# Performance work log

Measured on AMD Instinct MI355X. Metric: run time of the kernel, lower is better.

The kernel has to match this reference:

```python
import jax, jax.numpy as jnp
import numpy as np

B, S, E, P, K, H = 32, 512, 1024, 256, 3, 8
KERNELS = 4  # conv repeated KERNELS times then averaged -> identical to a single conv


def setup_inputs() -> dict:
    key = jax.random.key(0)
    ks = jax.random.split(key, 8)
    sc = 0.02
    x = jax.random.normal(ks[0], (B, S, E), jnp.float32)
    # lengths must satisfy 3 <= l <= S-1 so slice [1:l+1] and conv length l-2 are valid
    seq_length = jax.random.randint(ks[1], (B,), 16, S - 1)
    proj_w = jax.random.normal(ks[2], (E, P), jnp.float32) * sc
    proj_b = jnp.zeros((P,), jnp.float32)
    conv_w = jax.random.normal(ks[3], (P, P, K), jnp.float32) * sc  # (out, in, width)
    conv_b = jnp.zeros((P,), jnp.float32)
    attn_w = jax.random.normal(ks[4], (P, H * S), jnp.float32) * sc
    attn_b = jnp.zeros((H * S,), jnp.float32)
    c1_w = jax.random.normal(ks[5], (P, P // 2), jnp.float32) * sc
    c1_b = jnp.zeros((P // 2,), jnp.float32)
    c2_w = jax.random.normal(ks[6], (P // 2, 2), jnp.float32) * sc
    c2_b = jnp.zeros((2,), jnp.float32)
    return dict(x=x, seq_length=seq_length, proj_w=proj_w, proj_b=proj_b,
                conv_w=conv_w, conv_b=conv_b, attn_w=attn_w, attn_b=attn_b,
                c1_w=c1_w, c1_b=c1_b, c2_w=c2_w, c2_b=c2_b)


def _forward(x, seq_length, proj_w, proj_b, conv_w, conv_b, attn_w, attn_b,
             c1_w, c1_b, c2_w, c2_b):
    # projection: (B,S,E) -> (B,S,P)
    proj = jnp.einsum('bse,ep->bsp', x, proj_w) + proj_b
    proj_pc = jnp.transpose(proj, (0, 2, 1))  # (B,P,S)
    # original convs each sample over slice [1:l+1]; conv is local, so conv the
    # full slice [1:] once and mask invalid tail positions per sample.
    conv = jax.lax.conv_general_dilated(
        proj_pc[:, :, 1:], conv_w, window_strides=(1,), padding='VALID',
        dimension_numbers=('NCH', 'OIH', 'NCH'))  # (B,P,S-K)
    conv = jax.nn.relu(conv + conv_b[None, :, None])
    # sum of KERNELS identical relu(conv) outputs divided by KERNELS == conv (identity)
    m = S - K  # conv output length over slice [1:]
    l = seq_length[:, None]  # (B,1)
    valid = jnp.arange(m)[None, :] < (l - (K - 1))  # output j valid iff j < l-2
    conv = jnp.where(valid[:, None, :], conv, 0.0)
    # pad: position 0 zero, conv outputs at 1..l-2, zeros after -> (B,P,S)
    rep_conv = jnp.zeros((B, P, S), conv.dtype).at[:, :, 1:1 + m].set(conv)
    rep_conv = jnp.transpose(rep_conv, (0, 2, 1))  # (B,S,P)
    # attention: logits (B,S,H*S), softmax over the FULL H*S axis (original dim=1)
    logits = jnp.einsum('bsp,pk->bsk', rep_conv, attn_w) + attn_b
    attn = jax.nn.softmax(logits, axis=-1).reshape(B, S, H, S)
    # per sample: mean over heads, sum over query rows -> weights over key pos q
    w = attn.sum(axis=(1, 2)) / H  # (B,S)
    rep_attn = jnp.einsum('bq,bqp->bp', w, rep_conv)  # (B,P)
    h = jnp.einsum('bp,ph->bh', rep_attn, c1_w) + c1_b
    h = jnp.where(h > 0, h, 0.01 * h)  # LeakyReLU(0.01)
    cls = jnp.einsum('bh,hc->bc', h, c2_w) + c2_b
    return jax.nn.softmax(cls, axis=-1)


def reference(x, seq_length, proj_w, proj_b, conv_w, conv_b, attn_w, attn_b,
              c1_w, c1_b, c2_w, c2_b):
    probs = _forward(x, seq_length, proj_w, proj_b, conv_w, conv_b,
                     attn_w, attn_b, c1_w, c1_b, c2_w, c2_b)
    return probs, jnp.argmax(probs, axis=1)
```

## Files before the change

kernel.cpp:

```cpp
#include <hip/hip_runtime.h>
#include <hip/hip_fp8.h>

#define B_ 32
#define S_ 512
#define E_ 1024
#define P_ 256
#define HH 8

typedef __attribute__((ext_vector_type(8))) short bf16x8;
typedef __attribute__((ext_vector_type(8))) unsigned short us8;
typedef __attribute__((ext_vector_type(4))) unsigned short us4;
typedef __attribute__((ext_vector_type(16))) float f32x16;
typedef __attribute__((ext_vector_type(4))) float f32x4;
typedef __attribute__((ext_vector_type(8))) unsigned char u8x8;

#define SA 8.0f
#define SB 16.0f
#define SINV (1.0f / 128.0f)
#define LOG2E 1.44269504088896f
#define SINV2 (SINV * LOG2E)

static __device__ __forceinline__ unsigned short f2bf(float f) {
  union { float f; unsigned int u; } v;
  v.f = f;
  unsigned int r = (v.u + 0x7FFFu + ((v.u >> 16) & 1u)) >> 16;
  return (unsigned short)r;
}
static __device__ __forceinline__ float bf2f(unsigned short u) {
  union { unsigned int u; float f; } v;
  v.u = ((unsigned int)u) << 16;
  return v.f;
}
static __device__ __forceinline__ unsigned char f2fp8(float f) {
  return (unsigned char)__hip_cvt_float_to_fp8(f, __HIP_SATFINITE, __HIP_E4M3);
}

__global__ __launch_bounds__(256) void k_prep(const float* __restrict__ pw,
                                              const float* __restrict__ cw,
                                              const float* __restrict__ aw,
                                              unsigned short* __restrict__ pwB,
                                              unsigned short* __restrict__ wtB,
                                              unsigned char* __restrict__ awB8,
                                              float* __restrict__ zbase) {
  int bid = blockIdx.x;
  int t = threadIdx.x;
  if (bid < 160) {
    zbase[bid * 256 + t] = 0.f;
    return;
  }
  bid -= 160;
  if (bid < 128) {
    int g = bid >> 4, kc = (bid & 15) * 4 + (t >> 6);
    int l = t & 63;
    int n = g * 32 + (l & 31);
    int kbase = kc * 16 + (l >> 5) * 8;
    us8 v;
#pragma unroll
    for (int j = 0; j < 8; j++) v[j] = f2bf(pw[(size_t)(kbase + j) * P_ + n]);
    *(us8*)(pwB + ((size_t)g * 64 + kc) * 512 + l * 8) = v;
    return;
  }
  bid -= 128;
  if (bid < 96) {
    int g = bid / 12, kidx = (bid % 12) * 4 + (t >> 6);
    int l = t & 63;
    int o = g * 32 + (l & 31);
    int xb = kidx * 16 + (l >> 5) * 8;
    us8 v;
#pragma unroll
    for (int j = 0; j < 8; j++) {
      int x = xb + j;
      int k = x >> 8, i = x & 255;
      v[j] = f2bf(cw[(size_t)o * 768 + i * 3 + k]);
    }
    *(us8*)(wtB + ((size_t)g * 48 + kidx) * 512 + l * 8) = v;
    return;
  }
  bid -= 96;
  {
    int g = bid >> 1, ks = (bid & 1) * 4 + (t >> 6);
    int l = t & 63;
    int j0 = g * 16 + (l & 15);
    int kbase = ks * 32 + (l >> 4) * 8;
    u8x8 v;
#pragma unroll
    for (int j = 0; j < 8; j++) v[j] = f2fp8(aw[(size_t)(kbase + j) * 4096 + j0] * SB);
    *(u8x8*)(awB8 + ((size_t)g * 8 + ks) * 512 + l * 8) = v;
  }
}

__global__ __launch_bounds__(256) void k_swz8(const unsigned short* __restrict__ src,
                                              unsigned char* __restrict__ dst) {
  int g = blockIdx.x, ks = blockIdx.y * 4 + (threadIdx.x >> 6);
  int l = threadIdx.x & 63;
  us8 v = *(const us8*)(src + (size_t)(g * 16 + (l & 15)) * 256 + ks * 32 + (l >> 4) * 8);
  u8x8 o;
#pragma unroll
  for (int j = 0; j < 8; j++) o[j] = f2fp8(bf2f(v[j]) * SA);
  *(u8x8*)(dst + ((size_t)g * 8 + ks) * 512 + l * 8) = o;
}

__global__ __launch_bounds__(512) void k_proj_mfma(const float* __restrict__ x,
                                                   const unsigned short* __restrict__ pwB,
                                                   const float* __restrict__ pb,
                                                   unsigned short* __restrict__ proj16) {
  __shared__ unsigned short As[16 * 64 * 8];
  const int m0 = blockIdx.x * 64;
  const int t = threadIdx.x;
  const int w = t >> 6, lane = t & 63, ln31 = lane & 31, kh = lane >> 5;
  const int c0 = w * 32;

  f32x16 acc0, acc1;
#pragma unroll
  for (int r = 0; r < 16; r++) { acc0[r] = 0.f; acc1[r] = 0.f; }

  const unsigned short* bp = pwB + (size_t)w * 64 * 512 + lane * 8;

  for (int kc = 0; kc < E_; kc += 128) {
#pragma unroll
    for (int i = 0; i < 4; i++) {
      int c = t + i * 512;
      int row = c >> 5, pos = c & 31;
      float4 v = *(const float4*)(x + (size_t)(m0 + row) * E_ + kc + pos * 4);
      us4 h;
      h[0] = f2bf(v.x); h[1] = f2bf(v.y); h[2] = f2bf(v.z); h[3] = f2bf(v.w);
      *(us4*)&As[((pos >> 1) * 64 + row) * 8 + (pos & 1) * 4] = h;
    }
    __syncthreads();
    const int kcs = kc >> 4;
#pragma unroll
    for (int kk = 0; kk < 8; kk++) {
      bf16x8 a0 = *(const bf16x8*)&As[((2 * kk + kh) * 64 + ln31) * 8];
      bf16x8 a1 = *(const bf16x8*)&As[((2 * kk + kh) * 64 + 32 + ln31) * 8];
      bf16x8 b  = *(const bf16x8*)(bp + (size_t)(kcs + kk) * 512);
      acc0 = __builtin_amdgcn_mfma_f32_32x32x16_bf16(a0, b, acc0, 0, 0, 0);
      acc1 = __builtin_amdgcn_mfma_f32_32x32x16_bf16(a1, b, acc1, 0, 0, 0);
    }
    __syncthreads();
  }
  float pbv = pb[c0 + ln31];
#pragma unroll
  for (int r = 0; r < 16; r++) {
    int rl = (r & 3) + 8 * (r >> 2) + 4 * kh;
    proj16[(size_t)(m0 + rl) * P_ + c0 + ln31]      = f2bf(acc0[r] + pbv);
    proj16[(size_t)(m0 + 32 + rl) * P_ + c0 + ln31] = f2bf(acc1[r] + pbv);
  }
}

__global__ __launch_bounds__(512) void k_conv_mfma(const unsigned short* __restrict__ proj16,
                                                   const unsigned short* __restrict__ wtB,
                                                   const float* __restrict__ cb,
                                                   const int* __restrict__ seq,
                                                   unsigned short* __restrict__ rep16) {
  __shared__ unsigned short As[32 * 66 * 8];
  const int m0 = blockIdx.x * 64;
  const int bb = m0 >> 9, s0 = m0 & 511;
  const int t = threadIdx.x;
  const int w = t >> 6, lane = t & 63, ln31 = lane & 31, kh = lane >> 5;
  const int c0 = w * 32;

#pragma unroll
  for (int i = 0; i < 5; i++) {
    int c = t + i * 512;
    if (c < 2112) {
      int row = c >> 5, kk2 = c & 31;
      us8 v = {0, 0, 0, 0, 0, 0, 0, 0};
      if (s0 + row <= 511)
        v = *(const us8*)(proj16 + (size_t)(bb * S_ + s0 + row) * P_ + kk2 * 8);
      *(us8*)&As[(kk2 * 66 + row) * 8] = v;
    }
  }
  __syncthreads();

  f32x16 acc0, acc1;
#pragma unroll
  for (int r = 0; r < 16; r++) { acc0[r] = 0.f; acc1[r] = 0.f; }

  const unsigned short* bbase = wtB + (size_t)w * 48 * 512 + lane * 8;

#pragma unroll
  for (int k = 0; k < 3; k++) {
#pragma unroll
    for (int kk = 0; kk < 16; kk++) {
      bf16x8 a0 = *(const bf16x8*)&As[((2 * kk + kh) * 66 + k + ln31) * 8];
      bf16x8 a1 = *(const bf16x8*)&As[((2 * kk + kh) * 66 + k + 32 + ln31) * 8];
      bf16x8 b  = *(const bf16x8*)(bbase + (size_t)(k * 16 + kk) * 512);
      acc0 = __builtin_amdgcn_mfma_f32_32x32x16_bf16(a0, b, acc0, 0, 0, 0);
      acc1 = __builtin_amdgcn_mfma_f32_32x32x16_bf16(a1, b, acc1, 0, 0, 0);
    }
  }

  int l = seq[bb];
  float cbv = cb[c0 + ln31];
#pragma unroll
  for (int r = 0; r < 16; r++) {
    int rl = (r & 3) + 8 * (r >> 2) + 4 * kh;
    int s_a = s0 + rl, s_b = s0 + 32 + rl;
    float ma = (s_a >= 1 && s_a <= 509 && s_a < l - 1) ? 1.f : 0.f;
    float mb = (s_b >= 1 && s_b <= 509 && s_b < l - 1) ? 1.f : 0.f;
    rep16[(size_t)(m0 + rl) * P_ + c0 + ln31]      = f2bf(fmaxf(acc0[r] + cbv, 0.f) * ma);
    rep16[(size_t)(m0 + 32 + rl) * P_ + c0 + ln31] = f2bf(fmaxf(acc1[r] + cbv, 0.f) * mb);
  }
}

__global__ __launch_bounds__(256) void k_attn_mfma(const unsigned char* __restrict__ repF8,
                                                   const unsigned char* __restrict__ awB8,
                                                   const float* __restrict__ ab,
                                                   unsigned short* __restrict__ E16,
                                                   float* __restrict__ Z) {
  __shared__ __align__(16) unsigned char As8[16384];
  const int m0 = blockIdx.x * 64;
  const int q0 = blockIdx.y * 128;
  const int t = threadIdx.x;
  const int w = t >> 6, lane = t & 63;
  const int ln15 = lane & 15, l4 = lane >> 4;

  {
    const float4* src = (const float4*)(repF8 + (size_t)m0 * 256);
    float4* dst = (float4*)As8;
#pragma unroll
    for (int i = 0; i < 4; i++) dst[t + i * 256] = src[t + i * 256];
  }
  __syncthreads();

  const int qg = (q0 >> 5) + w;

  f32x4 ef[8];
#pragma unroll
  for (int i = 0; i < 8; i++) ef[i] = (f32x4){0.f, 0.f, 0.f, 0.f};

#pragma unroll 1
  for (int h = 0; h < HH; h++) {
    unsigned oz = 0;
    asm volatile("" : "+v"(oz));
    const unsigned char* bh = awB8 + (size_t)(h * 32 + qg * 2) * 8 * 512 + lane * 8;
    f32x4 acc[8];
#pragma unroll
    for (int i = 0; i < 8; i++) acc[i] = (f32x4){0.f, 0.f, 0.f, 0.f};
#pragma unroll
    for (int ks = 0; ks < 8; ks++) {
      long b0 = *(const long*)(bh + (size_t)ks * 512);
      long b1 = *(const long*)(bh + (size_t)(8 + ks) * 512);
#pragma unroll
      for (int rt = 0; rt < 4; rt++) {
        long a = *(const long*)&As8[(rt * 8 + ks) * 512 + lane * 8 + oz];
        acc[rt * 2 + 0] = __builtin_amdgcn_mfma_f32_16x16x32_fp8_fp8(a, b0, acc[rt * 2 + 0], 0, 0, 0);
        acc[rt * 2 + 1] = __builtin_amdgcn_mfma_f32_16x16x32_fp8_fp8(a, b1, acc[rt * 2 + 1], 0, 0, 0);
      }
    }
    float bias0 = ab[h * 512 + qg * 32 + ln15] * LOG2E;
    float bias1 = ab[h * 512 + qg * 32 + 16 + ln15] * LOG2E;
#pragma unroll
    for (int rt = 0; rt < 4; rt++)
#pragma unroll
      for (int r = 0; r < 4; r++) {
        ef[rt * 2 + 0][r] += __builtin_amdgcn_exp2f(acc[rt * 2 + 0][r] * SINV2 + bias0);
        ef[rt * 2 + 1][r] += __builtin_amdgcn_exp2f(acc[rt * 2 + 1][r] * SINV2 + bias1);
      }
  }

#pragma unroll
  for (int rt = 0; rt < 4; rt++)
#pragma unroll
    for (int r = 0; r < 4; r++) {
      int row = m0 + rt * 16 + l4 * 4 + r;
      E16[(size_t)row * 512 + qg * 32 + ln15]      = f2bf(ef[rt * 2 + 0][r]);
      E16[(size_t)row * 512 + qg * 32 + 16 + ln15] = f2bf(ef[rt * 2 + 1][r]);
    }

#pragma unroll
  for (int rt = 0; rt < 4; rt++)
#pragma unroll
    for (int r = 0; r < 4; r++) {
      float z = ef[rt * 2 + 0][r] + ef[rt * 2 + 1][r];
#pragma unroll
      for (int st = 8; st >= 1; st >>= 1) z += __shfl_xor(z, st, 64);
      if (ln15 == 0) atomicAdd(&Z[m0 + rt * 16 + l4 * 4 + r], z);
    }
}

__global__ __launch_bounds__(512) void k_w(const unsigned short* __restrict__ E16,
                                           const float* __restrict__ Z,
                                           float* __restrict__ wB) {
  __shared__ float rZ[64];
  int b = blockIdx.x, c = blockIdx.y, t = threadIdx.x;
  int s0 = c * 64;
  if (t < 64) rZ[t] = 1.0f / Z[b * 512 + s0 + t];
  __syncthreads();
  float acc = 0.f;
#pragma unroll 8
  for (int s = 0; s < 64; s++)
    acc += bf2f(E16[(size_t)(b * 512 + s0 + s) * 512 + t]) * rZ[s];
  atomicAdd(&wB[b * 512 + t], acc * (1.0f / HH));
}

__global__ __launch_bounds__(256) void k_final_a(const unsigned short* __restrict__ rep16,
                                                 const float* __restrict__ wB,
                                                 float* __restrict__ repA) {
  __shared__ float wS[64];
  int b = blockIdx.x, qc = blockIdx.y, t = threadIdx.x;
  if (t < 64) wS[t] = wB[b * 512 + qc * 64 + t];
  __syncthreads();
  int p0 = (t & 63) * 4, qo = t >> 6;
  float a0 = 0.f, a1 = 0.f, a2 = 0.f, a3 = 0.f;
  for (int q = qo; q < 64; q += 4) {
    us4 v = *(const us4*)(rep16 + (size_t)(b * 512 + qc * 64 + q) * 256 + p0);
    float wq = wS[q];
    a0 += wq * bf2f(v[0]); a1 += wq * bf2f(v[1]);
    a2 += wq * bf2f(v[2]); a3 += wq * bf2f(v[3]);
  }
  atomicAdd(&repA[b * 256 + p0 + 0], a0);
  atomicAdd(&repA[b * 256 + p0 + 1], a1);
  atomicAdd(&repA[b * 256 + p0 + 2], a2);
  atomicAdd(&repA[b * 256 + p0 + 3], a3);
}

__global__ __launch_bounds__(128) void k_final_b(const float* __restrict__ repA,
                                                 const float* __restrict__ c1w,
                                                 const float* __restrict__ c1b,
                                                 const float* __restrict__ c2w,
                                                 const float* __restrict__ c2b,
                                                 float* __restrict__ out) {
  __shared__ float hS[128];
  __shared__ float clsS[2];
  int b = blockIdx.x, t = threadIdx.x;
  float acc = c1b[t];
  for (int p = 0; p < 256; p++) acc += repA[b * 256 + p] * c1w[p * 128 + t];
  hS[t] = acc > 0.f ? acc : 0.01f * acc;
  __syncthreads();
  if (t < 2) {
    float a2 = c2b[t];
    for (int j = 0; j < 128; j++) a2 += hS[j] * c2w[j * 2 + t];
    clsS[t] = a2;
  }
  __syncthreads();
  if (t == 0) {
    float c0 = clsS[0], c1 = clsS[1];
    float m = fmaxf(c0, c1);
    float e0 = __expf(c0 - m), e1 = __expf(c1 - m);
    float inv = 1.0f / (e0 + e1);
    float p0 = e0 * inv, p1 = e1 * inv;
    out[b * 2 + 0] = p0;
    out[b * 2 + 1] = p1;
    out[B_ * 2 + b] = (p1 > p0) ? 1.0f : 0.0f;
  }
}

extern "C" void kernel_launch(void* const* d_in, const int* in_sizes, int n_in,
                              void* d_out, int out_size, void* d_ws, size_t ws_size,
                              hipStream_t stream) {
  const float* x   = (const float*)d_in[0];
  const int*   seq = (const int*)d_in[1];
  const float* pw  = (const float*)d_in[2];
  const float* pb  = (const float*)d_in[3];
  const float* cw  = (const float*)d_in[4];
  const float* cb  = (const float*)d_in[5];
  const float* aw  = (const float*)d_in[6];
  const float* ab  = (const float*)d_in[7];
  const float* c1w = (const float*)d_in[8];
  const float* c1b = (const float*)d_in[9];
  const float* c2w = (const float*)d_in[10];
  const float* c2b = (const float*)d_in[11];
  float* out = (float*)d_out;

  char* ws = (char*)d_ws;
  unsigned short* proj16 = (unsigned short*)(ws);
  unsigned short* E16    = (unsigned short*)(ws);
  unsigned short* rep16  = (unsigned short*)(ws + (size_t)16777216);
  unsigned char*  repF8  = (unsigned char*)(ws + (size_t)25165824);
  unsigned char*  awB8   = (unsigned char*)(ws + (size_t)29360128);
  unsigned short* pwB    = (unsigned short*)(ws + (size_t)30408704);
  unsigned short* wtB    = (unsigned short*)(ws + (size_t)30932992);
  float*          Z      = (float*)(ws + (size_t)31326208);
  float*          wB     = (float*)(ws + (size_t)31391744);
  float*          repA   = (float*)(ws + (size_t)31457280);

  k_prep<<<896, 256, 0, stream>>>(pw, cw, aw, pwB, wtB, awB8, Z);
  k_proj_mfma<<<256, 512, 0, stream>>>(x, pwB, pb, proj16);
  k_conv_mfma<<<256, 512, 0, stream>>>(proj16, wtB, cb, seq, rep16);
  k_swz8<<<dim3(1024, 2), 256, 0, stream>>>(rep16, repF8);
  k_attn_mfma<<<dim3(256, 4), 256, 0, stream>>>(repF8, awB8, ab, E16, Z);
  k_w<<<dim3(32, 8), 512, 0, stream>>>(E16, Z, wB);
  k_final_a<<<dim3(32, 8), 256, 0, stream>>>(rep16, wB, repA);
  k_final_b<<<32, 128, 0, stream>>>(repA, c1w, c1b, c2w, c2b, out);
}
```

Measured before the change: 213.9 us.

## Double-buffer attention weight tiles in LDS via async global_load_lds prefetch

The attention MFMA kernel now stages each head's fp8 weight slice into a double-buffered shared-memory area using direct global-to-LDS loads. It prefetches the next head's slice while the current head's MFMAs run, with per-wave `s_waitcnt vmcnt` gating instead of block barriers. The per-head bias values are also loaded into registers once before the loop. This is meant to hide global-load latency on the B operand. In exchange the kernel takes 64KB of extra LDS, which lowers occupancy, and the bias array is indexed by a runtime loop counter, which may force it into scratch or indexed register moves.

Result: no change. 216.4 us (+1.2%).

```diff
diff --git a/kernel.cpp b/kernel.cpp
--- a/kernel.cpp
+++ b/kernel.cpp
@@ -33,6 +33,11 @@
 }
 static __device__ __forceinline__ unsigned char f2fp8(float f) {
   return (unsigned char)__hip_cvt_float_to_fp8(f, __HIP_SATFINITE, __HIP_E4M3);
+}
+static __device__ __forceinline__ void gll16(const void* g, void* l) {
+  __builtin_amdgcn_global_load_lds(
+      (const __attribute__((address_space(1))) void*)g,
+      (__attribute__((address_space(3))) void*)l, 16, 0, 0);
 }
 
 __global__ __launch_bounds__(256) void k_prep(const float* __restrict__ pw,
@@ -209,11 +214,13 @@
                                                    unsigned short* __restrict__ E16,
                                                    float* __restrict__ Z) {
   __shared__ __align__(16) unsigned char As8[16384];
+  __shared__ __align__(16) unsigned char Bs[2][32768];
   const int m0 = blockIdx.x * 64;
   const int q0 = blockIdx.y * 128;
   const int t = threadIdx.x;
   const int w = t >> 6, lane = t & 63;
   const int ln15 = lane & 15, l4 = lane >> 4;
+  const int qg = (q0 >> 5) + w;
 
   {
     const float4* src = (const float4*)(repF8 + (size_t)m0 * 256);
@@ -221,9 +228,22 @@
 #pragma unroll
     for (int i = 0; i < 4; i++) dst[t + i * 256] = src[t + i * 256];
   }
-  __syncthreads();
-
-  const int qg = (q0 >> 5) + w;
+
+  float biasr[2][8];
+#pragma unroll
+  for (int h = 0; h < HH; h++) {
+    biasr[0][h] = ab[h * 512 + qg * 32 + ln15] * LOG2E;
+    biasr[1][h] = ab[h * 512 + qg * 32 + 16 + ln15] * LOG2E;
+    asm volatile("" : "+v"(biasr[0][h]), "+v"(biasr[1][h]));
+  }
+
+  {
+    const unsigned char* bs = awB8 + (size_t)(qg * 2) * 4096 + lane * 16;
+    unsigned char* bd = &Bs[0][0] + w * 8192;
+#pragma unroll
+    for (int i = 0; i < 8; i++) gll16(bs + i * 1024, bd + i * 1024);
+  }
+  __syncthreads();
 
   f32x4 ef[8];
 #pragma unroll
@@ -231,16 +251,27 @@
 
 #pragma unroll 1
   for (int h = 0; h < HH; h++) {
+    if (h < HH - 1) {
+      const unsigned char* bs = awB8 + (size_t)((h + 1) * 32 + qg * 2) * 4096 + lane * 16;
+      unsigned char* bd = &Bs[(h + 1) & 1][0] + w * 8192;
+#pragma unroll
+      for (int i = 0; i < 8; i++) gll16(bs + i * 1024, bd + i * 1024);
+      asm volatile("s_waitcnt vmcnt(8)" ::: "memory");
+    } else {
+      asm volatile("s_waitcnt vmcnt(0)" ::: "memory");
+    }
+    __builtin_amdgcn_sched_barrier(0);
+
     unsigned oz = 0;
     asm volatile("" : "+v"(oz));
-    const unsigned char* bh = awB8 + (size_t)(h * 32 + qg * 2) * 8 * 512 + lane * 8;
+    const unsigned char* bh = &Bs[h & 1][0] + w * 8192 + lane * 8;
     f32x4 acc[8];
 #pragma unroll
     for (int i = 0; i < 8; i++) acc[i] = (f32x4){0.f, 0.f, 0.f, 0.f};
 #pragma unroll
     for (int ks = 0; ks < 8; ks++) {
-      long b0 = *(const long*)(bh + (size_t)ks * 512);
-      long b1 = *(const long*)(bh + (size_t)(8 + ks) * 512);
+      long b0 = *(const long*)(bh + ks * 512);
+      long b1 = *(const long*)(bh + 4096 + ks * 512);
 #pragma unroll
       for (int rt = 0; rt < 4; rt++) {
         long a = *(const long*)&As8[(rt * 8 + ks) * 512 + lane * 8 + oz];
@@ -248,8 +279,8 @@
         acc[rt * 2 + 1] = __builtin_amdgcn_mfma_f32_16x16x32_fp8_fp8(a, b1, acc[rt * 2 + 1], 0, 0, 0);
       }
     }
-    float bias0 = ab[h * 512 + qg * 32 + ln15] * LOG2E;
-    float bias1 = ab[h * 512 + qg * 32 + 16 + ln15] * LOG2E;
+    float bias0 = biasr[0][h];
+    float bias1 = biasr[1][h];
 #pragma unroll
     for (int rt = 0; rt < 4; rt++)
 #pragma unroll
```

## Double-buffer projection GEMM A tile with register prefetch and XOR-swizzled LDS

Applied to the files above, without the earlier changes.

The projection kernel now prefetches the next 128-wide K chunk of x into registers while MFMAs consume the current LDS buffer. It then converts that chunk to bf16 and writes it into a second LDS buffer, leaving one barrier per iteration instead of two. The LDS layout also gains an XOR swizzle meant to reduce bank conflicts on the writes and the MFMA operand reads. The cost is double the LDS footprint and more live registers, which could lower occupancy.

After: 226.5 us. 1.06x slower.

```diff
diff --git a/kernel.cpp b/kernel.cpp
--- a/kernel.cpp
+++ b/kernel.cpp
@@ -100,44 +100,80 @@
   *(u8x8*)(dst + ((size_t)g * 8 + ks) * 512 + l * 8) = o;
 }
 
+static __device__ __forceinline__ int aidx(int q, int row, int half) {
+  return (((q * 64 + row) * 8) + half * 4) ^ (((q ^ (row >> 3)) & 7) << 3);
+}
+
 __global__ __launch_bounds__(512) void k_proj_mfma(const float* __restrict__ x,
                                                    const unsigned short* __restrict__ pwB,
                                                    const float* __restrict__ pb,
                                                    unsigned short* __restrict__ proj16) {
-  __shared__ unsigned short As[16 * 64 * 8];
+  __shared__ unsigned short As[2][16 * 64 * 8];
   const int m0 = blockIdx.x * 64;
   const int t = threadIdx.x;
   const int w = t >> 6, lane = t & 63, ln31 = lane & 31, kh = lane >> 5;
   const int c0 = w * 32;
+  const int rbase = t >> 5, pos = t & 31;
+  const int q = pos >> 1, half = pos & 1;
 
   f32x16 acc0, acc1;
 #pragma unroll
   for (int r = 0; r < 16; r++) { acc0[r] = 0.f; acc1[r] = 0.f; }
 
   const unsigned short* bp = pwB + (size_t)w * 64 * 512 + lane * 8;
-
-  for (int kc = 0; kc < E_; kc += 128) {
-#pragma unroll
-    for (int i = 0; i < 4; i++) {
-      int c = t + i * 512;
-      int row = c >> 5, pos = c & 31;
-      float4 v = *(const float4*)(x + (size_t)(m0 + row) * E_ + kc + pos * 4);
-      us4 h;
-      h[0] = f2bf(v.x); h[1] = f2bf(v.y); h[2] = f2bf(v.z); h[3] = f2bf(v.w);
-      *(us4*)&As[((pos >> 1) * 64 + row) * 8 + (pos & 1) * 4] = h;
-    }
-    __syncthreads();
-    const int kcs = kc >> 4;
+  const float* xbase = x + (size_t)(m0 + rbase) * E_ + pos * 4;
+
+  float4 v0, v1, v2, v3;
+  v0 = *(const float4*)(xbase);
+  v1 = *(const float4*)(xbase + 16 * E_);
+  v2 = *(const float4*)(xbase + 32 * E_);
+  v3 = *(const float4*)(xbase + 48 * E_);
+  {
+    us4 h;
+    h[0] = f2bf(v0.x); h[1] = f2bf(v0.y); h[2] = f2bf(v0.z); h[3] = f2bf(v0.w);
+    *(us4*)&As[0][aidx(q, rbase, half)] = h;
+    h[0] = f2bf(v1.x); h[1] = f2bf(v1.y); h[2] = f2bf(v1.z); h[3] = f2bf(v1.w);
+    *(us4*)&As[0][aidx(q, rbase + 16, half)] = h;
+    h[0] = f2bf(v2.x); h[1] = f2bf(v2.y); h[2] = f2bf(v2.z); h[3] = f2bf(v2.w);
+    *(us4*)&As[0][aidx(q, rbase + 32, half)] = h;
+    h[0] = f2bf(v3.x); h[1] = f2bf(v3.y); h[2] = f2bf(v3.z); h[3] = f2bf(v3.w);
+    *(us4*)&As[0][aidx(q, rbase + 48, half)] = h;
+  }
+  __syncthreads();
+
+  for (int k8 = 0; k8 < 8; k8++) {
+    const int cur = k8 & 1;
+    if (k8 < 7) {
+      const float* xs = xbase + (k8 + 1) * 128;
+      v0 = *(const float4*)(xs);
+      v1 = *(const float4*)(xs + 16 * E_);
+      v2 = *(const float4*)(xs + 32 * E_);
+      v3 = *(const float4*)(xs + 48 * E_);
+    }
 #pragma unroll
     for (int kk = 0; kk < 8; kk++) {
-      bf16x8 a0 = *(const bf16x8*)&As[((2 * kk + kh) * 64 + ln31) * 8];
-      bf16x8 a1 = *(const bf16x8*)&As[((2 * kk + kh) * 64 + 32 + ln31) * 8];
-      bf16x8 b  = *(const bf16x8*)(bp + (size_t)(kcs + kk) * 512);
+      const int qr = 2 * kk + kh;
+      bf16x8 a0 = *(const bf16x8*)&As[cur][aidx(qr, ln31, 0)];
+      bf16x8 a1 = *(const bf16x8*)&As[cur][aidx(qr, 32 + ln31, 0)];
+      bf16x8 b  = *(const bf16x8*)(bp + (size_t)(k8 * 8 + kk) * 512);
       acc0 = __builtin_amdgcn_mfma_f32_32x32x16_bf16(a0, b, acc0, 0, 0, 0);
       acc1 = __builtin_amdgcn_mfma_f32_32x32x16_bf16(a1, b, acc1, 0, 0, 0);
     }
+    if (k8 < 7) {
+      const int nxt = cur ^ 1;
+      us4 h;
+      h[0] = f2bf(v0.x); h[1] = f2bf(v0.y); h[2] = f2bf(v0.z); h[3] = f2bf(v0.w);
+      *(us4*)&As[nxt][aidx(q, rbase, half)] = h;
+      h[0] = f2bf(v1.x); h[1] = f2bf(v1.y); h[2] = f2bf(v1.z); h[3] = f2bf(v1.w);
+      *(us4*)&As[nxt][aidx(q, rbase + 16, half)] = h;
+      h[0] = f2bf(v2.x); h[1] = f2bf(v2.y); h[2] = f2bf(v2.z); h[3] = f2bf(v2.w);
+      *(us4*)&As[nxt][aidx(q, rbase + 32, half)] = h;
+      h[0] = f2bf(v3.x); h[1] = f2bf(v3.y); h[2] = f2bf(v3.z); h[3] = f2bf(v3.w);
+      *(us4*)&As[nxt][aidx(q, rbase + 48, half)] = h;
+    }
     __syncthreads();
   }
+
   float pbv = pb[c0 + ln31];
 #pragma unroll
   for (int r = 0; r < 16; r++) {
```
